# Optimization experiments

Hardware: AMD Instinct MI355X
Metric: run time of the kernel (lower is better)

## Reference

```python
import jax, jax.numpy as jnp
import numpy as np

EMB = 64
D = 2 * EMB          # 128, feature dim of R / hidden of attention MLP
B, L = 128, 4096     # batch, sequence length
N_ITER = 50          # bisection iterations (entmax_bisect default)


def entmax_bisect(X, alpha, n_iter=N_ITER):
    """alpha-entmax via bisection over the last axis. X: [B, L], alpha: [B, 1] (>1)."""
    am1 = alpha - 1.0
    Xs = X * am1
    d = X.shape[-1]
    inv = 1.0 / am1
    max_val = jnp.max(Xs, axis=-1, keepdims=True)
    tau_lo0 = max_val - 1.0                       # gp(1, alpha) = 1
    tau_hi = max_val - (1.0 / d) ** am1           # gp(1/d, alpha)

    def p(tau):
        return jnp.clip(Xs - tau, 0.0, None) ** inv

    f_lo = jnp.sum(p(tau_lo0), axis=-1, keepdims=True) - 1.0

    def body(i, carry):
        tau_lo, dm, _ = carry
        dm = dm * 0.5
        tau_m = tau_lo + dm
        f_m = jnp.sum(p(tau_m), axis=-1, keepdims=True) - 1.0
        tau_lo = jnp.where(f_m * f_lo >= 0, tau_m, tau_lo)
        return (tau_lo, dm, tau_m)

    _, _, tau_m = jax.lax.fori_loop(0, n_iter, body, (tau_lo0, tau_hi - tau_lo0, tau_lo0))
    p_m = p(tau_m)
    return p_m / jnp.sum(p_m, axis=-1, keepdims=True)  # ensure_sum_one


def setup_inputs() -> dict:
    key = jax.random.key(0)
    ks = jax.random.split(key, 9)
    s = 1.0 / np.sqrt(D)
    R = jax.random.normal(ks[0], (B, L, D), dtype=jnp.float32)
    alpha = 1.25 + 0.5 * jax.random.uniform(ks[1], (B, 1), dtype=jnp.float32)  # in (1.25, 1.75)
    target = jax.random.normal(ks[2], (B, 1, D), dtype=jnp.float32)
    Wr1 = s * jax.random.normal(ks[3], (D, D), dtype=jnp.float32)      # Linear(2E, 2E), no bias
    Wr2 = s * jax.random.normal(ks[4], (D, EMB), dtype=jnp.float32)    # Linear(E, 2E) (shape-fixed), no bias
    Wr3 = s * jax.random.normal(ks[5], (1, D), dtype=jnp.float32)      # Linear(2E, 1), no bias
    bias_r = s * jax.random.normal(ks[6], (D,), dtype=jnp.float32)
    Wf_w = s * jax.random.normal(ks[7], (EMB, D), dtype=jnp.float32)   # Linear(2E, E)
    Wf_b = s * jax.random.normal(ks[8], (EMB,), dtype=jnp.float32)
    return {"R": R, "alpha": alpha, "target": target, "Wr1": Wr1, "Wr2": Wr2,
            "Wr3": Wr3, "bias_r": bias_r, "Wf_w": Wf_w, "Wf_b": Wf_b}


def reference(R, alpha, target, Wr1, Wr2, Wr3, bias_r, Wf_w, Wf_b):
    # q = Wf(target): [B, 1, E]
    q = jnp.einsum('btd,ed->bte', target, Wf_w) + Wf_b
    # additive attention score: Wr3 @ relu(Wr1 k + Wr2 q + b): [B, L]
    h = jax.nn.relu(jnp.einsum('bld,ed->ble', R, Wr1)
                    + jnp.einsum('bte,de->btd', q, Wr2)
                    + bias_r)
    scores = jnp.einsum('bld,d->bl', h, Wr3[0])
    # entmax sparsification over the sequence axis
    a = entmax_bisect(scores, alpha)
    # weighted sum of v = R: [B, D]
    res = jnp.einsum('bl,bld->bd', a, R)
    res = jax.nn.selu(res)
    res = res / jnp.linalg.norm(res, axis=-1, keepdims=True)
    return res
```

## Files before the change

kernel.cpp:

```cpp
#include <hip/hip_runtime.h>
#include <hip/hip_bf16.h>

#define B_ 128
#define L_ 4096
#define D_ 128
#define E_ 64

typedef __attribute__((ext_vector_type(8))) short short8;
typedef __attribute__((ext_vector_type(4))) float floatx4;

static __device__ __forceinline__ unsigned short f2bf(float x) {
  __hip_bfloat16 h = __float2bfloat16(x);
  union { __hip_bfloat16 h; unsigned short u; } c; c.h = h; return c.u;
}
static __device__ __forceinline__ float bf2f(unsigned short u) {
  union { unsigned short u; __hip_bfloat16 h; } c; c.u = u; return __bfloat162float(c.h);
}

__global__ __launch_bounds__(128) void pass_a(
    const float* __restrict__ target, const float* __restrict__ Wr2,
    const float* __restrict__ bias_r, const float* __restrict__ Wf_w,
    const float* __restrict__ Wf_b, float* __restrict__ cvec) {
  const int b = blockIdx.x, t = threadIdx.x;
  __shared__ float tg[D_];
  __shared__ float q[E_];
  tg[t] = target[b * D_ + t];
  __syncthreads();
  if (t < E_) {
    float s = Wf_b[t];
    #pragma unroll 8
    for (int d = 0; d < D_; ++d) s += tg[d] * Wf_w[t * D_ + d];
    q[t] = s;
  }
  __syncthreads();
  float s = bias_r[t];
  #pragma unroll 8
  for (int e = 0; e < E_; ++e) s += q[e] * Wr2[t * E_ + e];
  cvec[b * D_ + t] = s;
}

__global__ __launch_bounds__(256) void wr1_split(const float* __restrict__ Wr1,
    unsigned short* __restrict__ hi, unsigned short* __restrict__ lo) {
  int t = blockIdx.x * 256 + threadIdx.x;
  int j = t & 7, lane = (t >> 3) & 63, ks = (t >> 9) & 3, nt = t >> 11;
  int e = nt * 16 + (lane & 15);
  int d = ks * 32 + (lane >> 4) * 8 + j;
  float x = Wr1[e * D_ + d];
  unsigned short h = f2bf(x);
  hi[t] = h;
  lo[t] = f2bf(x - bf2f(h));
}

__global__ __launch_bounds__(256, 2) void pass_b(
    const float* __restrict__ R, const unsigned short* __restrict__ Whi,
    const unsigned short* __restrict__ Wlo, const float* __restrict__ cvec,
    const float* __restrict__ Wr3, float* __restrict__ scores) {
  __shared__ __align__(16) unsigned short sAhi[16384];
  __shared__ __align__(16) unsigned short sAlo[16384];
  const int b = blockIdx.x >> 5;
  const int lt = blockIdx.x & 31;
  const int t = threadIdx.x;
  const int wave = t >> 6, lane = t & 63;
  const int col = lane & 15, quad = lane >> 4;

  const float* Rbase = R + ((size_t)b * L_ + (size_t)lt * 128) * D_;
  #pragma unroll
  for (int i = 0; i < 8; ++i) {
    const int mt = wave * 2 + (i >> 2);
    const int ks = i & 3;
    const int row = mt * 16 + (lane & 15);
    const int c0 = ks * 32 + (lane >> 4) * 8;
    const float4* p = (const float4*)(Rbase + (size_t)row * D_ + c0);
    float4 v0 = p[0], v1 = p[1];
    float vv[8] = {v0.x, v0.y, v0.z, v0.w, v1.x, v1.y, v1.z, v1.w};
    union { unsigned short u[8]; short8 v; } H, Lo;
    #pragma unroll
    for (int j = 0; j < 8; ++j) {
      unsigned short h = f2bf(vv[j]);
      H.u[j] = h;
      Lo.u[j] = f2bf(vv[j] - bf2f(h));
    }
    const int base = ((mt * 4 + ks) * 64 + lane) * 8;
    *(short8*)(sAhi + base) = H.v;
    *(short8*)(sAlo + base) = Lo.v;
  }

  short8 bh[2][4], bl[2][4];
  #pragma unroll
  for (int n = 0; n < 2; ++n)
    #pragma unroll
    for (int ks = 0; ks < 4; ++ks) {
      int off = (((wave * 2 + n) * 4 + ks) * 64 + lane) * 8;
      bh[n][ks] = *(const short8*)(Whi + off);
      bl[n][ks] = *(const short8*)(Wlo + off);
    }

  floatx4 acc[8][2];
  #pragma unroll
  for (int mt = 0; mt < 8; ++mt)
    #pragma unroll
    for (int n = 0; n < 2; ++n) acc[mt][n] = (floatx4){0.f, 0.f, 0.f, 0.f};

  __syncthreads();

  #pragma unroll
  for (int mt = 0; mt < 8; ++mt) {
    #pragma unroll
    for (int ks = 0; ks < 4; ++ks) {
      int ai = ((mt * 4 + ks) * 64 + lane) * 8;
      short8 ah = *(const short8*)(sAhi + ai);
      short8 al = *(const short8*)(sAlo + ai);
      #pragma unroll
      for (int n = 0; n < 2; ++n) {
        acc[mt][n] = __builtin_amdgcn_mfma_f32_16x16x32_bf16(ah, bh[n][ks], acc[mt][n], 0, 0, 0);
        acc[mt][n] = __builtin_amdgcn_mfma_f32_16x16x32_bf16(al, bh[n][ks], acc[mt][n], 0, 0, 0);
        acc[mt][n] = __builtin_amdgcn_mfma_f32_16x16x32_bf16(ah, bl[n][ks], acc[mt][n], 0, 0, 0);
      }
    }
  }

  float w3[2], cb[2];
  #pragma unroll
  for (int n = 0; n < 2; ++n) {
    int e = (wave * 2 + n) * 16 + col;
    w3[n] = Wr3[e];
    cb[n] = cvec[b * D_ + e];
  }
  float part[8][4];
  #pragma unroll
  for (int mt = 0; mt < 8; ++mt)
    #pragma unroll
    for (int r = 0; r < 4; ++r) {
      float s = 0.f;
      #pragma unroll
      for (int n = 0; n < 2; ++n)
        s += w3[n] * fmaxf(acc[mt][n][r] + cb[n], 0.f);
      s += __shfl_xor(s, 1, 64);
      s += __shfl_xor(s, 2, 64);
      s += __shfl_xor(s, 4, 64);
      s += __shfl_xor(s, 8, 64);
      part[mt][r] = s;
    }
  __syncthreads();
  float* red = (float*)sAhi;
  if (col == 0) {
    #pragma unroll
    for (int mt = 0; mt < 8; ++mt)
      #pragma unroll
      for (int r = 0; r < 4; ++r)
        red[wave * 128 + mt * 16 + quad * 4 + r] = part[mt][r];
  }
  __syncthreads();
  if (t < 128) {
    float s = (red[t] + red[128 + t]) + (red[256 + t] + red[384 + t]);
    scores[(size_t)b * L_ + lt * 128 + t] = s;
  }
}

__global__ __launch_bounds__(512) void pass_cd(
    const float* __restrict__ scores, const float* __restrict__ alpha,
    const float* __restrict__ R, float* __restrict__ out) {
  const int b = blockIdx.x, t = threadIdx.x;
  const int wave = t >> 6, lane = t & 63;
  __shared__ float sred[2][8];
  __shared__ unsigned short sidx[L_];
  __shared__ float sw[L_];
  __shared__ float ppart[512];
  __shared__ int scnt;
  const float am1 = alpha[b] - 1.0f;
  const float inv = 1.0f / am1;
  const float* S = scores + (size_t)b * L_;
  float Xs[8];
  #pragma unroll
  for (int i = 0; i < 8; ++i) Xs[i] = S[i * 512 + t] * am1;
  if (t == 0) scnt = 0;

  float mx = Xs[0];
  #pragma unroll
  for (int i = 1; i < 8; ++i) mx = fmaxf(mx, Xs[i]);
  #pragma unroll
  for (int m = 32; m >= 1; m >>= 1) mx = fmaxf(mx, __shfl_xor(mx, m, 64));
  if (lane == 0) sred[0][wave] = mx;
  __syncthreads();
  mx = sred[0][0];
  #pragma unroll
  for (int w = 1; w < 8; ++w) mx = fmaxf(mx, sred[0][w]);

  float tau_lo = mx - 1.0f;
  float tau_hi = mx - exp2f(-12.0f * am1);
  float dm = tau_hi - tau_lo;

  int pc = 1;
  auto sumP = [&](float tau) -> float {
    const int par = pc & 1;
    ++pc;
    float s = 0.f;
    #pragma unroll
    for (int i = 0; i < 8; ++i) {
      float u = Xs[i] - tau;
      if (u > 0.f) s += exp2f(inv * __log2f(u));
    }
    #pragma unroll
    for (int m = 32; m >= 1; m >>= 1) s += __shfl_xor(s, m, 64);
    if (lane == 0) sred[par][wave] = s;
    __syncthreads();
    float r = sred[par][0];
    #pragma unroll
    for (int w = 1; w < 8; ++w) r += sred[par][w];
    return r;
  };

  const float f_lo = sumP(tau_lo) - 1.0f;
  float tau_m = tau_lo;
  for (int it = 0; it < 40; ++it) {
    dm *= 0.5f;
    tau_m = tau_lo + dm;
    float f_m = sumP(tau_m) - 1.0f;
    if (f_m * f_lo >= 0.f) tau_lo = tau_m;
  }

  float p[8];
  float s = 0.f;
  #pragma unroll
  for (int i = 0; i < 8; ++i) {
    float u = Xs[i] - tau_m;
    p[i] = (u > 0.f) ? exp2f(inv * __log2f(u)) : 0.f;
    s += p[i];
  }
  {
    const int par = pc & 1;
    ++pc;
    float ss = s;
    #pragma unroll
    for (int m = 32; m >= 1; m >>= 1) ss += __shfl_xor(ss, m, 64);
    if (lane == 0) sred[par][wave] = ss;
    __syncthreads();
    s = sred[par][0];
    #pragma unroll
    for (int w = 1; w < 8; ++w) s += sred[par][w];
  }
  const float rs = 1.0f / s;
  #pragma unroll
  for (int i = 0; i < 8; ++i) {
    if (p[i] > 0.f) {
      int pos = atomicAdd(&scnt, 1);
      sidx[pos] = (unsigned short)(i * 512 + t);
      sw[pos] = p[i] * rs;
    }
  }
  __syncthreads();
  const int n = scnt;

  const float* Rb = R + (size_t)b * L_ * D_;
  const int g = t >> 7, c = t & 127;
  float acc = 0.f;
  int k = g;
  for (; k + 4 < n; k += 8) {
    int i0 = sidx[k], i1 = sidx[k + 4];
    float w0 = sw[k], w1 = sw[k + 4];
    acc += w0 * Rb[(size_t)i0 * D_ + c] + w1 * Rb[(size_t)i1 * D_ + c];
  }
  for (; k < n; k += 4) acc += sw[k] * Rb[(size_t)sidx[k] * D_ + c];
  __syncthreads();
  ppart[t] = acc;
  __syncthreads();
  float r = 0.f;
  if (t < 128) {
    float a2 = (ppart[t] + ppart[t + 128]) + (ppart[t + 256] + ppart[t + 384]);
    const float sc = 1.0507009873554805f, al = 1.6732632423543772f;
    r = a2 > 0.f ? sc * a2 : sc * al * (expf(a2) - 1.0f);
  }
  float q = r * r;
  #pragma unroll
  for (int m = 32; m >= 1; m >>= 1) q += __shfl_xor(q, m, 64);
  if (lane == 0) sred[0][wave] = q;
  __syncthreads();
  if (t < 128) {
    float nrm = sqrtf(sred[0][0] + sred[0][1]);
    out[b * D_ + t] = r / nrm;
  }
}

extern "C" void kernel_launch(void* const* d_in, const int* in_sizes, int n_in,
                              void* d_out, int out_size, void* d_ws, size_t ws_size,
                              hipStream_t stream) {
  const float* R      = (const float*)d_in[0];
  const float* alpha  = (const float*)d_in[1];
  const float* target = (const float*)d_in[2];
  const float* Wr1    = (const float*)d_in[3];
  const float* Wr2    = (const float*)d_in[4];
  const float* Wr3    = (const float*)d_in[5];
  const float* bias_r = (const float*)d_in[6];
  const float* Wf_w   = (const float*)d_in[7];
  const float* Wf_b   = (const float*)d_in[8];
  float* out = (float*)d_out;

  char* ws = (char*)d_ws;
  float* cvec          = (float*)ws;
  unsigned short* whi  = (unsigned short*)(ws + 65536);
  unsigned short* wlo  = (unsigned short*)(ws + 98304);
  float* scores        = (float*)(ws + 131072);

  hipLaunchKernelGGL(pass_a, dim3(B_), dim3(128), 0, stream,
                     target, Wr2, bias_r, Wf_w, Wf_b, cvec);
  hipLaunchKernelGGL(wr1_split, dim3(64), dim3(256), 0, stream, Wr1, whi, wlo);
  hipLaunchKernelGGL(pass_b, dim3(B_ * 32), dim3(256), 0, stream,
                     R, whi, wlo, cvec, Wr3, scores);
  hipLaunchKernelGGL(pass_cd, dim3(B_), dim3(512), 0, stream,
                     scores, alpha, R, out);
}
```

Measured before the change: 458.1 us.

## Fuse query projection and Wr1 split into score kernel, cut bisection iterations

Removes the separate pass_a and wr1_split launches. Each pass_b block now recomputes the per-batch query/bias vector and splits Wr1 into bf16 hi/lo parts itself, using bit truncation instead of round-to-nearest conversion. Bisection iterations drop from 40 to 24, and the normalisation by the probability sum is folded into the final output, which removes one barrier pass over the sparse list. The trade-offs are redundant per-block work (the GEMV runs in all 32 tiles of each batch), slightly different rounding, and a coarser entmax threshold that could affect accuracy.

```diff
diff --git a/kernel.cpp b/kernel.cpp
--- a/kernel.cpp
+++ b/kernel.cpp
@@ -9,77 +9,48 @@
 typedef __attribute__((ext_vector_type(8))) short short8;
 typedef __attribute__((ext_vector_type(4))) float floatx4;
 
-static __device__ __forceinline__ unsigned short f2bf(float x) {
-  __hip_bfloat16 h = __float2bfloat16(x);
-  union { __hip_bfloat16 h; unsigned short u; } c; c.h = h; return c.u;
-}
-static __device__ __forceinline__ float bf2f(unsigned short u) {
-  union { unsigned short u; __hip_bfloat16 h; } c; c.u = u; return __bfloat162float(c.h);
-}
-
-__global__ __launch_bounds__(128) void pass_a(
-    const float* __restrict__ target, const float* __restrict__ Wr2,
+static __device__ __forceinline__ void split_trunc(float x, unsigned short& hs,
+                                                   unsigned short& ls) {
+  unsigned int bx = __float_as_uint(x);
+  float hf = __uint_as_float(bx & 0xffff0000u);
+  hs = (unsigned short)(bx >> 16);
+  float lo = x - hf;
+  ls = (unsigned short)(__float_as_uint(lo) >> 16);
+}
+
+__global__ __launch_bounds__(256, 2) void pass_b(
+    const float* __restrict__ R, const float* __restrict__ alpha,
+    const float* __restrict__ target, const float* __restrict__ Wr1,
+    const float* __restrict__ Wr2, const float* __restrict__ Wr3,
     const float* __restrict__ bias_r, const float* __restrict__ Wf_w,
-    const float* __restrict__ Wf_b, float* __restrict__ cvec) {
-  const int b = blockIdx.x, t = threadIdx.x;
-  __shared__ float tg[D_];
-  __shared__ float q[E_];
-  tg[t] = target[b * D_ + t];
-  __syncthreads();
-  if (t < E_) {
-    float s = Wf_b[t];
-    #pragma unroll 8
-    for (int d = 0; d < D_; ++d) s += tg[d] * Wf_w[t * D_ + d];
-    q[t] = s;
-  }
-  __syncthreads();
-  float s = bias_r[t];
-  #pragma unroll 8
-  for (int e = 0; e < E_; ++e) s += q[e] * Wr2[t * E_ + e];
-  cvec[b * D_ + t] = s;
-}
-
-__global__ __launch_bounds__(256) void wr1_split(const float* __restrict__ Wr1,
-    unsigned short* __restrict__ hi, unsigned short* __restrict__ lo) {
-  int t = blockIdx.x * 256 + threadIdx.x;
-  int j = t & 7, lane = (t >> 3) & 63, ks = (t >> 9) & 3, nt = t >> 11;
-  int e = nt * 16 + (lane & 15);
-  int d = ks * 32 + (lane >> 4) * 8 + j;
-  float x = Wr1[e * D_ + d];
-  unsigned short h = f2bf(x);
-  hi[t] = h;
-  lo[t] = f2bf(x - bf2f(h));
-}
-
-__global__ __launch_bounds__(256, 2) void pass_b(
-    const float* __restrict__ R, const unsigned short* __restrict__ Whi,
-    const unsigned short* __restrict__ Wlo, const float* __restrict__ cvec,
-    const float* __restrict__ Wr3, float* __restrict__ scores) {
+    const float* __restrict__ Wf_b, float* __restrict__ scores) {
   __shared__ __align__(16) unsigned short sAhi[16384];
   __shared__ __align__(16) unsigned short sAlo[16384];
+  __shared__ float tg[D_];
+  __shared__ float qv[E_];
+  __shared__ float scvec[D_];
+
   const int b = blockIdx.x >> 5;
   const int lt = blockIdx.x & 31;
   const int t = threadIdx.x;
   const int wave = t >> 6, lane = t & 63;
   const int col = lane & 15, quad = lane >> 4;
 
+  if (t < D_) tg[t] = target[b * D_ + t];
+
   const float* Rbase = R + ((size_t)b * L_ + (size_t)lt * 128) * D_;
   #pragma unroll
   for (int i = 0; i < 8; ++i) {
     const int mt = wave * 2 + (i >> 2);
     const int ks = i & 3;
-    const int row = mt * 16 + (lane & 15);
-    const int c0 = ks * 32 + (lane >> 4) * 8;
+    const int row = mt * 16 + col;
+    const int c0 = ks * 32 + quad * 8;
     const float4* p = (const float4*)(Rbase + (size_t)row * D_ + c0);
     float4 v0 = p[0], v1 = p[1];
     float vv[8] = {v0.x, v0.y, v0.z, v0.w, v1.x, v1.y, v1.z, v1.w};
     union { unsigned short u[8]; short8 v; } H, Lo;
     #pragma unroll
-    for (int j = 0; j < 8; ++j) {
-      unsigned short h = f2bf(vv[j]);
-      H.u[j] = h;
-      Lo.u[j] = f2bf(vv[j] - bf2f(h));
-    }
+    for (int j = 0; j < 8; ++j) split_trunc(vv[j], H.u[j], Lo.u[j]);
     const int base = ((mt * 4 + ks) * 64 + lane) * 8;
     *(short8*)(sAhi + base) = H.v;
     *(short8*)(sAlo + base) = Lo.v;
@@ -90,9 +61,16 @@
   for (int n = 0; n < 2; ++n)
     #pragma unroll
     for (int ks = 0; ks < 4; ++ks) {
-      int off = (((wave * 2 + n) * 4 + ks) * 64 + lane) * 8;
-      bh[n][ks] = *(const short8*)(Whi + off);
-      bl[n][ks] = *(const short8*)(Wlo + off);
+      const int e = (wave * 2 + n) * 16 + col;
+      const int c0 = ks * 32 + quad * 8;
+      const float4* p = (const float4*)(Wr1 + e * D_ + c0);
+      float4 v0 = p[0], v1 = p[1];
+      float vv[8] = {v0.x, v0.y, v0.z, v0.w, v1.x, v1.y, v1.z, v1.w};
+      union { unsigned short u[8]; short8 v; } H, Lo;
+      #pragma unroll
+      for (int j = 0; j < 8; ++j) split_trunc(vv[j], H.u[j], Lo.u[j]);
+      bh[n][ks] = H.v;
+      bl[n][ks] = Lo.v;
     }
 
   floatx4 acc[8][2];
@@ -103,11 +81,25 @@
 
   __syncthreads();
 
+  if (t < E_) {
+    float s = Wf_b[t];
+    #pragma unroll 8
+    for (int d = 0; d < D_; ++d) s += tg[d] * Wf_w[t * D_ + d];
+    qv[t] = s;
+  }
+  __syncthreads();
+  if (t < D_) {
+    float s = bias_r[t];
+    #pragma unroll 8
+    for (int e = 0; e < E_; ++e) s += qv[e] * Wr2[t * E_ + e];
+    scvec[t] = s;
+  }
+
   #pragma unroll
   for (int mt = 0; mt < 8; ++mt) {
     #pragma unroll
     for (int ks = 0; ks < 4; ++ks) {
-      int ai = ((mt * 4 + ks) * 64 + lane) * 8;
+      const int ai = ((mt * 4 + ks) * 64 + lane) * 8;
       short8 ah = *(const short8*)(sAhi + ai);
       short8 al = *(const short8*)(sAlo + ai);
       #pragma unroll
@@ -119,12 +111,14 @@
     }
   }
 
+  __syncthreads();
+
   float w3[2], cb[2];
   #pragma unroll
   for (int n = 0; n < 2; ++n) {
-    int e = (wave * 2 + n) * 16 + col;
+    const int e = (wave * 2 + n) * 16 + col;
     w3[n] = Wr3[e];
-    cb[n] = cvec[b * D_ + e];
+    cb[n] = scvec[e];
   }
   float part[8][4];
   #pragma unroll
@@ -141,7 +135,6 @@
       s += __shfl_xor(s, 8, 64);
       part[mt][r] = s;
     }
-  __syncthreads();
   float* red = (float*)sAhi;
   if (col == 0) {
     #pragma unroll
@@ -187,8 +180,7 @@
   for (int w = 1; w < 8; ++w) mx = fmaxf(mx, sred[0][w]);
 
   float tau_lo = mx - 1.0f;
-  float tau_hi = mx - exp2f(-12.0f * am1);
-  float dm = tau_hi - tau_lo;
+  float dm = (mx - exp2f(-12.0f * am1)) - tau_lo;
 
   int pc = 1;
   auto sumP = [&](float tau) -> float {
@@ -212,61 +204,55 @@
 
   const float f_lo = sumP(tau_lo) - 1.0f;
   float tau_m = tau_lo;
-  for (int it = 0; it < 40; ++it) {
+  for (int it = 0; it < 24; ++it) {
     dm *= 0.5f;
     tau_m = tau_lo + dm;
     float f_m = sumP(tau_m) - 1.0f;
     if (f_m * f_lo >= 0.f) tau_lo = tau_m;
   }
 
-  float p[8];
   float s = 0.f;
   #pragma unroll
   for (int i = 0; i < 8; ++i) {
     float u = Xs[i] - tau_m;
-    p[i] = (u > 0.f) ? exp2f(inv * __log2f(u)) : 0.f;
-    s += p[i];
+    if (u > 0.f) {
+      float p = exp2f(inv * __log2f(u));
+      s += p;
+      int pos = atomicAdd(&scnt, 1);
+      sidx[pos] = (unsigned short)(i * 512 + t);
+      sw[pos] = p;
+    }
   }
   {
     const int par = pc & 1;
     ++pc;
-    float ss = s;
-    #pragma unroll
-    for (int m = 32; m >= 1; m >>= 1) ss += __shfl_xor(ss, m, 64);
-    if (lane == 0) sred[par][wave] = ss;
+    #pragma unroll
+    for (int m = 32; m >= 1; m >>= 1) s += __shfl_xor(s, m, 64);
+    if (lane == 0) sred[par][wave] = s;
     __syncthreads();
     s = sred[par][0];
     #pragma unroll
     for (int w = 1; w < 8; ++w) s += sred[par][w];
   }
+  const int ns = scnt;
   const float rs = 1.0f / s;
-  #pragma unroll
-  for (int i = 0; i < 8; ++i) {
-    if (p[i] > 0.f) {
-      int pos = atomicAdd(&scnt, 1);
-      sidx[pos] = (unsigned short)(i * 512 + t);
-      sw[pos] = p[i] * rs;
-    }
-  }
-  __syncthreads();
-  const int n = scnt;
 
   const float* Rb = R + (size_t)b * L_ * D_;
   const int g = t >> 7, c = t & 127;
   float acc = 0.f;
   int k = g;
-  for (; k + 4 < n; k += 8) {
+  for (; k + 4 < ns; k += 8) {
     int i0 = sidx[k], i1 = sidx[k + 4];
     float w0 = sw[k], w1 = sw[k + 4];
     acc += w0 * Rb[(size_t)i0 * D_ + c] + w1 * Rb[(size_t)i1 * D_ + c];
   }
-  for (; k < n; k += 4) acc += sw[k] * Rb[(size_t)sidx[k] * D_ + c];
+  for (; k < ns; k += 4) acc += sw[k] * Rb[(size_t)sidx[k] * D_ + c];
   __syncthreads();
   ppart[t] = acc;
   __syncthreads();
   float r = 0.f;
   if (t < 128) {
-    float a2 = (ppart[t] + ppart[t + 128]) + (ppart[t + 256] + ppart[t + 384]);
+    float a2 = ((ppart[t] + ppart[t + 128]) + (ppart[t + 256] + ppart[t + 384])) * rs;
     const float sc = 1.0507009873554805f, al = 1.6732632423543772f;
     r = a2 > 0.f ? sc * a2 : sc * al * (expf(a2) - 1.0f);
   }
@@ -295,17 +281,10 @@
   const float* Wf_b   = (const float*)d_in[8];
   float* out = (float*)d_out;
 
-  char* ws = (char*)d_ws;
-  float* cvec          = (float*)ws;
-  unsigned short* whi  = (unsigned short*)(ws + 65536);
-  unsigned short* wlo  = (unsigned short*)(ws + 98304);
-  float* scores        = (float*)(ws + 131072);
-
-  hipLaunchKernelGGL(pass_a, dim3(B_), dim3(128), 0, stream,
-                     target, Wr2, bias_r, Wf_w, Wf_b, cvec);
-  hipLaunchKernelGGL(wr1_split, dim3(64), dim3(256), 0, stream, Wr1, whi, wlo);
+  float* scores = (float*)d_ws;
+
   hipLaunchKernelGGL(pass_b, dim3(B_ * 32), dim3(256), 0, stream,
-                     R, whi, wlo, cvec, Wr3, scores);
+                     R, alpha, target, Wr1, Wr2, Wr3, bias_r, Wf_w, Wf_b, scores);
   hipLaunchKernelGGL(pass_cd, dim3(B_), dim3(512), 0, stream,
                      scores, alpha, R, out);
 }
```

New measurement: 493.2 us. +7.7%, slower.
